# Kernel optimization log

Hardware: AMD Instinct MI355X
Metric: run time of the kernel (lower is better)

The kernel has to match this reference:

```python
import jax, jax.numpy as jnp
import numpy as np

IMAGE_H, IMAGE_W = 256, 704
Z, Y, X = 128, 8, 128
BOUNDS = (-50.0, 50.0, -5.0, 5.0, -50.0, 50.0)
CENTROID = (0.0, 1.0, 0.0)
EPS_MEAN = 1e-6
EPS_DEPTH = 1e-4


def _compose_rt(R, t):
    M = jnp.zeros(R.shape[:-2] + (4, 4), R.dtype)
    M = M.at[..., :3, :3].set(R)
    M = M.at[..., :3, 3].set(t)
    M = M.at[..., 3, 3].set(1.0)
    return M


def _safe_inverse(M):
    R = M[..., :3, :3]
    t = M[..., :3, 3]
    Rt = jnp.swapaxes(R, -1, -2)
    return _compose_rt(Rt, -jnp.einsum('...ij,...j->...i', Rt, t))


def _apply_4x4(M, xyz):
    # M: (...,4,4), xyz: (...,N,3) -> (...,N,3)
    return jnp.einsum('...ij,...nj->...ni', M[..., :3, :3], xyz) + M[..., None, :3, 3]


def _xyz_camA():
    # Mem2Ref of gridcloud3d: x_ref = x_mem*vox + MIN + vox/2 (bounds shifted by centroid)
    xmin = BOUNDS[0] + CENTROID[0]; xmax = BOUNDS[1] + CENTROID[0]
    ymin = BOUNDS[2] + CENTROID[1]; ymax = BOUNDS[3] + CENTROID[1]
    zmin = BOUNDS[4] + CENTROID[2]; zmax = BOUNDS[5] + CENTROID[2]
    vx = (xmax - xmin) / X; vy = (ymax - ymin) / Y; vz = (zmax - zmin) / Z
    zz, yy, xx = jnp.meshgrid(jnp.arange(Z, dtype=jnp.float32),
                              jnp.arange(Y, dtype=jnp.float32),
                              jnp.arange(X, dtype=jnp.float32), indexing='ij')
    x = xx * vx + xmin + vx / 2.0
    y = yy * vy + ymin + vy / 2.0
    z = zz * vz + zmin + vz / 2.0
    return jnp.stack([x, y, z], -1).reshape(Z * Y * X, 3)  # mem order (Z,Y,X)


def _bilinear_sample(img, px, py):
    # img: (C,H,W); px,py: (N,) pixel coords; zeros padding (grid_sample align_corners=False)
    C, H, W = img.shape
    x0 = jnp.floor(px); y0 = jnp.floor(py)
    dx = px - x0; dy = py - y0
    x0i = x0.astype(jnp.int32); y0i = y0.astype(jnp.int32)
    flat = img.reshape(C, H * W)

    def gather(yi, xi, w):
        inb = (xi >= 0) & (xi < W) & (yi >= 0) & (yi < H)
        idx = jnp.clip(yi, 0, H - 1) * W + jnp.clip(xi, 0, W - 1)
        return flat[:, idx] * (w * inb.astype(img.dtype))

    return (gather(y0i, x0i, (1 - dx) * (1 - dy))
            + gather(y0i, x0i + 1, dx * (1 - dy))
            + gather(y0i + 1, x0i, (1 - dx) * dy)
            + gather(y0i + 1, x0i + 1, dx * dy))  # (C,N)


def _forward(cam_feat, camera2ego, cam_intrinsic, conv_w):
    B, S, C, Hf, Wf = cam_feat.shape
    # velo_T_cams = merge_rt(camera2ego R, t); cam0_T_camXs = inv(velo_T_cams[:,0]) @ velo_T_cams
    velo_T_cams = _compose_rt(camera2ego[..., :3, :3], camera2ego[..., :3, 3])
    cam0_T_velo = _safe_inverse(velo_T_cams[:, 0])
    cam0_T_camXs = jnp.einsum('bij,bsjk->bsik', cam0_T_velo, velo_T_cams)
    camXs_T_cam0 = _safe_inverse(cam0_T_camXs)
    # scale_intrinsics with sy = Hf/H*0.284, sx = Wf/W*0.44
    sy = Hf / float(IMAGE_H) * 0.284
    sx = Wf / float(IMAGE_W) * 0.44
    fx = cam_intrinsic[..., 0, 0] * sx
    fy = cam_intrinsic[..., 1, 1] * sy
    cx = cam_intrinsic[..., 0, 2] * sx
    cy = cam_intrinsic[..., 1, 2] * sy
    K = jnp.zeros((B, S, 4, 4), cam_feat.dtype)
    K = K.at[..., 0, 0].set(fx).at[..., 1, 1].set(fy)
    K = K.at[..., 0, 2].set(cx).at[..., 1, 2].set(cy)
    K = K.at[..., 2, 2].set(1.0).at[..., 3, 3].set(1.0)
    pixB_T_cam0 = jnp.einsum('bsij,bsjk->bsik', K, camXs_T_cam0)

    xyz = _xyz_camA()  # (N,3), N = Z*Y*X
    xyz_camB = _apply_4x4(camXs_T_cam0, xyz[None, None])  # (B,S,N,3)
    z_cam = xyz_camB[..., 2]
    xyz_pix = _apply_4x4(pixB_T_cam0, xyz[None, None])
    depth = jnp.maximum(xyz_pix[..., 2], EPS_DEPTH)
    x_pix = xyz_pix[..., 0] / depth
    y_pix = xyz_pix[..., 1] / depth
    valid = ((x_pix > -0.5) & (x_pix < Wf - 0.5)
             & (y_pix > -0.5) & (y_pix < Hf - 0.5)
             & (z_cam > 0.0)).astype(cam_feat.dtype)
    # normalize_grid2d (clamp [-2,2]) then grid_sample align_corners=False unnormalize
    gx = jnp.clip(2.0 * x_pix / (Wf - 1) - 1.0, -2.0, 2.0)
    gy = jnp.clip(2.0 * y_pix / (Hf - 1) - 1.0, -2.0, 2.0)
    px = ((gx + 1.0) * Wf - 1.0) / 2.0
    py = ((gy + 1.0) * Hf - 1.0) / 2.0

    feats = cam_feat.reshape(B * S, C, Hf, Wf)
    vals = jax.vmap(_bilinear_sample)(feats, px.reshape(B * S, -1), py.reshape(B * S, -1))
    vals = vals.reshape(B, S, C, -1) * valid[:, :, None, :]  # (B,S,C,N)
    mask = (jnp.abs(vals) > 0).astype(vals.dtype)
    feat_mem = jnp.sum(vals * mask, axis=1) / (EPS_MEAN + jnp.sum(mask, axis=1))  # (B,C,N)
    feat_mem = feat_mem.reshape(B, C, Z, Y, X)

    # BEV compress: permute(0,1,3,2,4) -> (B, C*Y, Z, X), conv3x3 (no bias), InstanceNorm2d, GELU
    feat_bev = jnp.transpose(feat_mem, (0, 1, 3, 2, 4)).reshape(B, C * Y, Z, X)
    out = jax.lax.conv_general_dilated(feat_bev, conv_w, (1, 1), ((1, 1), (1, 1)),
                                       dimension_numbers=('NCHW', 'OIHW', 'NCHW'))
    mu = jnp.mean(out, axis=(2, 3), keepdims=True)
    var = jnp.var(out, axis=(2, 3), keepdims=True)
    out = (out - mu) / jnp.sqrt(var + 1e-5)
    return jax.nn.gelu(out, approximate=False)


def setup_inputs() -> dict:
    key = jax.random.key(0)
    k1, k2, k3 = jax.random.split(key, 3)
    B, S, C, Hf, Wf = 1, 6, 128, 32, 88
    cam_feat = jax.random.normal(k1, (B, S, C, Hf, Wf), jnp.float32)
    # rigid camera2ego: yaw rotations about the y axis + small translations
    yaws = jnp.arange(S, dtype=jnp.float32) * (2.0 * jnp.pi / S)
    c, s = jnp.cos(yaws), jnp.sin(yaws)
    zr, on = jnp.zeros_like(c), jnp.ones_like(c)
    R = jnp.stack([jnp.stack([c, zr, s], -1),
                   jnp.stack([zr, on, zr], -1),
                   jnp.stack([-s, zr, c], -1)], -2)  # (S,3,3)
    t = jax.random.normal(k2, (S, 3), jnp.float32) * 0.5
    cam2ego = jnp.zeros((B, S, 4, 4), jnp.float32)
    cam2ego = cam2ego.at[0, :, :3, :3].set(R).at[0, :, :3, 3].set(t).at[0, :, 3, 3].set(1.0)
    K = jnp.zeros((B, S, 4, 4), jnp.float32)
    K = K.at[..., 0, 0].set(600.0).at[..., 1, 1].set(600.0)
    K = K.at[..., 0, 2].set(352.0).at[..., 1, 2].set(128.0)
    K = K.at[..., 2, 2].set(1.0).at[..., 3, 3].set(1.0)
    conv_w = jax.random.normal(k3, (128, 128 * Y, 3, 3), jnp.float32) / np.sqrt(128 * Y * 9.0).astype(np.float32)
    return {"cam_feat": cam_feat, "camera2ego": cam2ego, "cam_intrinsic": K, "conv_w": conv_w}


def reference(cam_feat, camera2ego, cam_intrinsic, conv_w):
    return _forward(cam_feat, camera2ego, cam_intrinsic, conv_w)
```

## Files before the change

### kernel.cpp

```cpp
#include <hip/hip_runtime.h>
#include <hip/hip_bf16.h>
#include <math.h>

#define HF 32
#define WF 88
#define NCAM 6
#define CC 128
#define ZD 128
#define YD 8
#define XD 128

using f32x4  = __attribute__((ext_vector_type(4))) float;
using bf16x8 = __attribute__((ext_vector_type(8))) short;
using h2     = __attribute__((ext_vector_type(2))) _Float16;

#if defined(__has_builtin)
#if __has_builtin(__builtin_amdgcn_fdot2)
#define HAVE_FDOT2 1
#endif
#endif
__device__ __forceinline__ float fdot2f(h2 a, h2 b, float c) {
#ifdef HAVE_FDOT2
  return __builtin_amdgcn_fdot2(a, b, c, false);
#else
  return c + (float)a[0] * (float)b[0] + (float)a[1] * (float)b[1];
#endif
}

#define OFF_P    0ull
#define OFF_W    512ull
#define OFF_CAMT (OFF_W + 2359296ull)
#define OFF_F    (OFF_CAMT + 8650752ull)
#define OFF_CONV (OFF_F + 34611200ull)

__global__ __launch_bounds__(256) void k_pre(const float* __restrict__ feat,
                                             const float* __restrict__ conv_w,
                                             const float* __restrict__ cam2ego,
                                             const float* __restrict__ intr,
                                             unsigned* __restrict__ camT2,
                                             __hip_bfloat16* __restrict__ wp,
                                             float* __restrict__ P) {
  __shared__ float tile[128 * 89];
  const int b = blockIdx.x;
  const int t = threadIdx.x;
  if (b < 192) {
    const int s = b >> 5;
    const int hrow = b & 31;
    for (int idx = t; idx < 128 * 88; idx += 256) {
      const int c = idx / 88;
      const int w = idx - c * 88;
      tile[c * 89 + w] = feat[((size_t)(s * CC + c) * HF + hrow) * WF + w];
    }
    __syncthreads();
    unsigned* dst = camT2 + (size_t)(s * 32 + hrow) * 87 * 128;
    for (int idx = t; idx < 87 * 128; idx += 256) {
      const int px = idx >> 7;
      const int c = idx & 127;
      union { _Float16 h[2]; unsigned u; } pr;
      pr.h[0] = (_Float16)tile[c * 89 + px];
      pr.h[1] = (_Float16)tile[c * 89 + px + 1];
      dst[px * 128 + c] = pr.u;
    }
  } else if (b < 704) {
    const int tt = (b - 192) * 256 + t;
    float v[9];
    #pragma unroll
    for (int d = 0; d < 9; d++) v[d] = conv_w[(size_t)tt * 9 + d];
    #pragma unroll
    for (int d = 0; d < 9; d++) wp[(size_t)d * 131072 + tt] = __float2bfloat16(v[d]);
  } else {
    const int s = t;
    if (s >= NCAM) return;
    const float* M0 = cam2ego;
    const float* Ms = cam2ego + s * 16;
    float Rb[9], tb[3];
    for (int i = 0; i < 3; i++)
      for (int j = 0; j < 3; j++) {
        float v = 0.f;
        for (int k = 0; k < 3; k++) v += Ms[k * 4 + i] * M0[k * 4 + j];
        Rb[i * 3 + j] = v;
      }
    for (int i = 0; i < 3; i++) {
      float v = 0.f;
      for (int k = 0; k < 3; k++) v += Ms[k * 4 + i] * (M0[k * 4 + 3] - Ms[k * 4 + 3]);
      tb[i] = v;
    }
    const float* Ks = intr + s * 16;
    const float sx = (float)WF / 704.0f * 0.44f;
    const float sy = (float)HF / 256.0f * 0.284f;
    const float fx = Ks[0] * sx, fy = Ks[5] * sy;
    const float cx = Ks[2] * sx, cy = Ks[6] * sy;
    float* p = P + s * 12;
    for (int j = 0; j < 3; j++) p[j]     = fx * Rb[j]     + cx * Rb[6 + j];
    p[3]  = fx * tb[0] + cx * tb[2];
    for (int j = 0; j < 3; j++) p[4 + j] = fy * Rb[3 + j] + cy * Rb[6 + j];
    p[7]  = fy * tb[1] + cy * tb[2];
    for (int j = 0; j < 3; j++) p[8 + j] = Rb[6 + j];
    p[11] = tb[2];
  }
}

__global__ __launch_bounds__(256) void k2_sample(const unsigned* __restrict__ camT2,
                                                 const float* __restrict__ P,
                                                 __hip_bfloat16* __restrict__ F) {
  const int wv = threadIdx.x >> 6;
  const int l  = threadIdx.x & 63;
  const int cell = blockIdx.x * 4 + wv;
  const int bz = cell / 130;
  const int bx = cell - bz * 130;
  const int zi = bz - 1, xi = bx - 1;
  __hip_bfloat16* Fb = F + (size_t)cell * 1024;

  if (zi < 0 || zi >= ZD || xi < 0 || xi >= XD) {
    const uint4 z4 = {0u, 0u, 0u, 0u};
    *reinterpret_cast<uint4*>(Fb + (2 * l) * 8)     = z4;
    *reinterpret_cast<uint4*>(Fb + (2 * l + 1) * 8) = z4;
    return;
  }

  int offA = 0, offB = 0;
  unsigned pwA = 0, pwB = 0;
  bool vflag = false;
  if (l < 48) {
    const int y = l / 6, s = l - y * 6;
    const float* pp = P + s * 12;
    const float vx = 100.0f / 128.0f;
    const float xw = xi * vx - 50.0f + vx * 0.5f;
    const float zw = zi * vx - 50.0f + vx * 0.5f;
    const float yw = y * 1.25f - 4.0f + 0.625f;
    const float zc = pp[8] * xw + pp[9] * yw + pp[10] * zw + pp[11];
    const float xp = pp[0] * xw + pp[1] * yw + pp[2] * zw + pp[3];
    const float yp = pp[4] * xw + pp[5] * yw + pp[6] * zw + pp[7];
    const float dep = fmaxf(zc, 1e-4f);
    const float pxf = xp / dep, pyf = yp / dep;
    const bool valid = (pxf > -0.5f && pxf < (float)WF - 0.5f &&
                        pyf > -0.5f && pyf < (float)HF - 0.5f && zc > 0.0f);
    const float px = pxf * ((float)WF / (float)(WF - 1)) - 0.5f;
    const float py = pyf * ((float)HF / (float)(HF - 1)) - 0.5f;
    const float fx0 = floorf(px), fy0 = floorf(py);
    const float ddx = px - fx0, ddy = py - fy0;
    const int x0i = (int)fx0, y0i = (int)fy0;
    const float vf = valid ? 1.0f : 0.0f;
    const float wxl = (1.0f - ddx) * vf, wxr = ddx * vf;
    int pxi; float sl, sr;
    if (x0i >= 0 && x0i <= 86)      { pxi = x0i; sl = wxl; sr = wxr; }
    else if (x0i == -1)             { pxi = 0;   sl = wxr; sr = 0.f; }
    else if (x0i == 87)             { pxi = 86;  sl = 0.f; sr = wxl; }
    else                            { pxi = 0;   sl = 0.f; sr = 0.f; }
    const float fA = ((unsigned)y0i < (unsigned)HF) ? (1.0f - ddy) : 0.0f;
    const float fB = ((unsigned)(y0i + 1) < (unsigned)HF) ? ddy : 0.0f;
    const int rowA = min(max(y0i, 0), HF - 1);
    const int rowB = min(max(y0i + 1, 0), HF - 1);
    offA = ((s * HF + rowA) * 87 + pxi) * 128;
    offB = ((s * HF + rowB) * 87 + pxi) * 128;
    union { _Float16 h[2]; unsigned u; } wa, wb;
    wa.h[0] = (_Float16)(sl * fA); wa.h[1] = (_Float16)(sr * fA);
    wb.h[0] = (_Float16)(sl * fB); wb.h[1] = (_Float16)(sr * fB);
    pwA = wa.u; pwB = wb.u;
    vflag = ((sl + sr) * (fA + fB)) > 0.0f;
  }
  const unsigned long long m = __ballot(vflag);

  float accA[8], accB[8];
  #pragma unroll
  for (int y = 0; y < 8; y++) { accA[y] = 0.f; accB[y] = 0.f; }

  #pragma unroll
  for (int y = 0; y < 8; y++) {
    unsigned ms = (unsigned)((m >> (6 * y)) & 63ull);
    const int c = __popc(ms);
    while (ms) {
      const int s = __builtin_ctz(ms);
      ms &= ms - 1;
      const int src = y * 6 + s;
      const int oA = __shfl(offA, src);
      const int oB = __shfl(offB, src);
      const unsigned uwA = (unsigned)__shfl((int)pwA, src);
      const unsigned uwB = (unsigned)__shfl((int)pwB, src);
      const uint2 av = *reinterpret_cast<const uint2*>(camT2 + oA + 2 * l);
      const uint2 bv = *reinterpret_cast<const uint2*>(camT2 + oB + 2 * l);
      const h2 wa = __builtin_bit_cast(h2, uwA);
      const h2 wb = __builtin_bit_cast(h2, uwB);
      accA[y] = fdot2f(__builtin_bit_cast(h2, av.x), wa, accA[y]);
      accB[y] = fdot2f(__builtin_bit_cast(h2, av.y), wa, accB[y]);
      accA[y] = fdot2f(__builtin_bit_cast(h2, bv.x), wb, accA[y]);
      accB[y] = fdot2f(__builtin_bit_cast(h2, bv.y), wb, accB[y]);
    }
    const float inv = 1.0f / (1e-6f + (float)c);
    accA[y] *= inv;
    accB[y] *= inv;
  }

  union { __hip_bfloat16 h[8]; uint4 u; } pA, pB;
  #pragma unroll
  for (int y = 0; y < 8; y++) {
    pA.h[y] = __float2bfloat16(accA[y]);
    pB.h[y] = __float2bfloat16(accB[y]);
  }
  *reinterpret_cast<uint4*>(Fb + (2 * l) * 8)     = pA.u;
  *reinterpret_cast<uint4*>(Fb + (2 * l + 1) * 8) = pB.u;
}

__device__ __forceinline__ void load_lds16(const void* g, void* l) {
  __builtin_amdgcn_global_load_lds(
      (const __attribute__((address_space(1))) unsigned int*)g,
      (__attribute__((address_space(3))) unsigned int*)l, 16, 0, 0);
}

#define K3_NT 72

__global__ __launch_bounds__(512) void k3_gemm(const __hip_bfloat16* __restrict__ F,
                                               const __hip_bfloat16* __restrict__ Wp,
                                               float* __restrict__ out0,
                                               float* __restrict__ out1) {
  const int orig = (blockIdx.x & 7) * 32 + (blockIdx.x >> 3);
  const int z = orig & 127;
  const int h = orig >> 7;
  const int ciH = h << 9;
  const int tid = threadIdx.x;
  const int w = tid >> 6;
  const int l = tid & 63;
  const int kk = w >> 2;
  const int wq = w & 3;
  const int wm = wq >> 1;
  const int wn = wq & 1;
  __shared__ __hip_bfloat16 lds[4][16384];

  f32x4 acc[4][4];
  #pragma unroll
  for (int m = 0; m < 4; m++)
    #pragma unroll
    for (int n = 0; n < 4; n++)
      acc[m][n] = (f32x4){0.f, 0.f, 0.f, 0.f};

  auto stage_A = [&](int kt) {
    const int buf = kt & 3;
    const int d = kt >> 3;
    const int dz = d / 3, dx = d - dz * 3;
    const int ci0 = ciH + ((kt & 7) << 6);
    const int zbase = (z + dz) * 130 + dx;
    #pragma unroll
    for (int i = 0; i < 2; i++) {
      const int n = w * 128 + i * 64 + l;
      const int row = n >> 3;
      const int q = (n & 7) ^ (row & 7);
      const __hip_bfloat16* src = F + ((size_t)(zbase + row) << 10) + ci0 + (q << 3);
      load_lds16(src, &lds[buf][(w * 128 + i * 64) * 8]);
    }
  };
  auto stage_B = [&](int kt) {
    const int buf = kt & 3;
    const int d = kt >> 3;
    const int ci0 = ciH + ((kt & 7) << 6);
    #pragma unroll
    for (int i = 0; i < 2; i++) {
      const int n = w * 128 + i * 64 + l;
      const int co = n >> 3;
      const int q = (n & 7) ^ (co & 7);
      const __hip_bfloat16* src = Wp + ((size_t)d << 17) + ((size_t)co << 10) + ci0 + (q << 3);
      load_lds16(src, &lds[buf][8192 + (w * 128 + i * 64) * 8]);
    }
  };

  const int r16 = l & 15;
  const int hi = l >> 4;
  const int cslot = kk * 4 + hi;

  auto step = [&](int t, bool doStage, int wcode) {
    const int buf = t & 3;
    bf16x8 a[4], b[4];
    #pragma unroll
    for (int m = 0; m < 4; m++) {
      const int r = wm * 64 + m * 16 + r16;
      const int slot = cslot ^ (r & 7);
      a[m] = *reinterpret_cast<const bf16x8*>(&lds[buf][r * 64 + slot * 8]);
    }
    #pragma unroll
    for (int n = 0; n < 2; n++) {
      const int co = wn * 64 + n * 16 + r16;
      const int slot = cslot ^ (co & 7);
      b[n] = *reinterpret_cast<const bf16x8*>(&lds[buf][8192 + co * 64 + slot * 8]);
    }
    if (doStage) stage_A(t + 3);
    __builtin_amdgcn_s_barrier();
    __builtin_amdgcn_s_setprio(1);
    #pragma unroll
    for (int m = 0; m < 4; m++) {
      acc[m][0] = __builtin_amdgcn_mfma_f32_16x16x32_bf16(a[m], b[0], acc[m][0], 0, 0, 0);
      acc[m][1] = __builtin_amdgcn_mfma_f32_16x16x32_bf16(a[m], b[1], acc[m][1], 0, 0, 0);
    }
    __builtin_amdgcn_s_setprio(0);
    __builtin_amdgcn_s_barrier();
    #pragma unroll
    for (int n = 2; n < 4; n++) {
      const int co = wn * 64 + n * 16 + r16;
      const int slot = cslot ^ (co & 7);
      b[n] = *reinterpret_cast<const bf16x8*>(&lds[buf][8192 + co * 64 + slot * 8]);
    }
    if (doStage) stage_B(t + 3);
    __builtin_amdgcn_s_barrier();
    __builtin_amdgcn_s_setprio(1);
    #pragma unroll
    for (int m = 0; m < 4; m++) {
      acc[m][2] = __builtin_amdgcn_mfma_f32_16x16x32_bf16(a[m], b[2], acc[m][2], 0, 0, 0);
      acc[m][3] = __builtin_amdgcn_mfma_f32_16x16x32_bf16(a[m], b[3], acc[m][3], 0, 0, 0);
    }
    __builtin_amdgcn_s_setprio(0);
    if (wcode == 8)      asm volatile("s_waitcnt vmcnt(8)" ::: "memory");
    else if (wcode == 4) asm volatile("s_waitcnt vmcnt(4)" ::: "memory");
    else if (wcode == 0) asm volatile("s_waitcnt vmcnt(0)" ::: "memory");
    __builtin_amdgcn_s_barrier();
  };

  stage_A(0); stage_B(0); stage_A(1); stage_B(1); stage_A(2); stage_B(2);
  asm volatile("s_waitcnt vmcnt(8)" ::: "memory");
  __builtin_amdgcn_s_barrier();

  for (int t = 0; t < K3_NT - 3; ++t) step(t, true, 8);
  step(K3_NT - 3, false, 4);
  step(K3_NT - 2, false, 0);
  step(K3_NT - 1, false, -1);

  float* red = reinterpret_cast<float*>(&lds[0][0]);
  if (kk == 1) {
    float* dst = red + wq * 4096;
    #pragma unroll
    for (int m = 0; m < 4; m++)
      #pragma unroll
      for (int n = 0; n < 4; n++)
        *reinterpret_cast<f32x4*>(&dst[(m * 4 + n) * 256 + l * 4]) = acc[m][n];
  }
  __syncthreads();
  if (kk == 0) {
    const float* srcr = red + wq * 4096;
    float* outP = h ? out1 : out0;
    #pragma unroll
    for (int m = 0; m < 4; m++) {
      const int xr = wm * 64 + m * 16 + hi * 4;
      #pragma unroll
      for (int n = 0; n < 4; n++) {
        f32x4 o = *reinterpret_cast<const f32x4*>(&srcr[(m * 4 + n) * 256 + l * 4]);
        f32x4 r = acc[m][n] + o;
        const int co = wn * 64 + n * 16 + r16;
        *reinterpret_cast<f32x4*>(&outP[((size_t)co << 14) + (z << 7) + xr]) = r;
      }
    }
  }
}

__device__ __forceinline__ float gelu_exact(float x) {
  return 0.5f * x * (1.0f + erff(x * 0.70710678118654752440f));
}

__global__ __launch_bounds__(1024) void k4_ln(const float* __restrict__ c0,
                                              const float* __restrict__ c1,
                                              float* __restrict__ outp) {
  const int co = blockIdx.x;
  const int t = threadIdx.x;
  const float4* p0 = reinterpret_cast<const float4*>(c0 + ((size_t)co << 14));
  const float4* p1 = reinterpret_cast<const float4*>(c1 + ((size_t)co << 14));
  float4 v[4];
  float s = 0.f, s2 = 0.f;
  #pragma unroll
  for (int i = 0; i < 4; i++) {
    float4 a = p0[t + (i << 10)];
    float4 b = p1[t + (i << 10)];
    float4 r;
    r.x = a.x + b.x; r.y = a.y + b.y; r.z = a.z + b.z; r.w = a.w + b.w;
    v[i] = r;
    s  += r.x + r.y + r.z + r.w;
    s2 += r.x * r.x + r.y * r.y + r.z * r.z + r.w * r.w;
  }
  #pragma unroll
  for (int off = 32; off > 0; off >>= 1) {
    s  += __shfl_down(s, off);
    s2 += __shfl_down(s2, off);
  }
  __shared__ float red[32];
  __shared__ float mb[2];
  const int wv = t >> 6, ln = t & 63;
  if (ln == 0) { red[wv] = s; red[wv + 16] = s2; }
  __syncthreads();
  if (t == 0) {
    float S = 0.f, S2 = 0.f;
    #pragma unroll
    for (int i = 0; i < 16; i++) { S += red[i]; S2 += red[i + 16]; }
    float mu = S * (1.0f / 16384.0f);
    float var = S2 * (1.0f / 16384.0f) - mu * mu;
    mb[0] = mu;
    mb[1] = 1.0f / sqrtf(var + 1e-5f);
  }
  __syncthreads();
  const float mu = mb[0], inv = mb[1];
  float4* op = reinterpret_cast<float4*>(outp + ((size_t)co << 14));
  #pragma unroll
  for (int i = 0; i < 4; i++) {
    float4 x = v[i];
    float4 r;
    r.x = gelu_exact((x.x - mu) * inv);
    r.y = gelu_exact((x.y - mu) * inv);
    r.z = gelu_exact((x.z - mu) * inv);
    r.w = gelu_exact((x.w - mu) * inv);
    op[t + (i << 10)] = r;
  }
}

extern "C" void kernel_launch(void* const* d_in, const int* in_sizes, int n_in,
                              void* d_out, int out_size, void* d_ws, size_t ws_size,
                              hipStream_t stream) {
  const float* cam_feat = (const float*)d_in[0];
  const float* cam2ego  = (const float*)d_in[1];
  const float* intr     = (const float*)d_in[2];
  const float* conv_w   = (const float*)d_in[3];
  float* out = (float*)d_out;
  char* ws = (char*)d_ws;

  float*          P     = (float*)(ws + OFF_P);
  __hip_bfloat16* Wp    = (__hip_bfloat16*)(ws + OFF_W);
  unsigned*       camT2 = (unsigned*)(ws + OFF_CAMT);
  __hip_bfloat16* F     = (__hip_bfloat16*)(ws + OFF_F);
  float*          conv0 = (float*)(ws + OFF_CONV);
  float*          conv1 = (float*)(ws + OFF_CAMT);

  hipLaunchKernelGGL(k_pre, dim3(705), dim3(256), 0, stream,
                     cam_feat, conv_w, cam2ego, intr, camT2, Wp, P);
  hipLaunchKernelGGL(k2_sample, dim3(4225), dim3(256), 0, stream, camT2, P, F);
  hipLaunchKernelGGL(k3_gemm, dim3(256), dim3(512), 0, stream, F, Wp, conv0, conv1);
  hipLaunchKernelGGL(k4_ln, dim3(128), dim3(1024), 0, stream, conv0, conv1, out);
}
```

Baseline: 95.69 us.

## Split sampling cells across two waves and software-pipeline gathers

Each grid cell's eight Y levels are now split between two wavefronts, four levels each, and the grid size is doubled. The per-level gather loop uses readlane instead of shuffles and prefetches the next camera's feature rows before accumulating the current one. The aim is more parallelism and overlap of gather latency with the fdot2 work in the bilinear sampling kernel. In exchange each wave stores narrower 8-byte chunks instead of 16-byte ones, and the per-cell projection work is repeated across the two waves.

```diff
diff --git a/kernel.cpp b/kernel.cpp
--- a/kernel.cpp
+++ b/kernel.cpp
@@ -105,24 +105,26 @@
                                                  __hip_bfloat16* __restrict__ F) {
   const int wv = threadIdx.x >> 6;
   const int l  = threadIdx.x & 63;
-  const int cell = blockIdx.x * 4 + wv;
+  const int cell = blockIdx.x * 2 + (wv >> 1);
+  const int yh = wv & 1;
   const int bz = cell / 130;
   const int bx = cell - bz * 130;
   const int zi = bz - 1, xi = bx - 1;
   __hip_bfloat16* Fb = F + (size_t)cell * 1024;
 
   if (zi < 0 || zi >= ZD || xi < 0 || xi >= XD) {
-    const uint4 z4 = {0u, 0u, 0u, 0u};
-    *reinterpret_cast<uint4*>(Fb + (2 * l) * 8)     = z4;
-    *reinterpret_cast<uint4*>(Fb + (2 * l + 1) * 8) = z4;
+    const ushort4 z4 = {0, 0, 0, 0};
+    *reinterpret_cast<ushort4*>(Fb + (2 * l) * 8 + yh * 4)     = z4;
+    *reinterpret_cast<ushort4*>(Fb + (2 * l + 1) * 8 + yh * 4) = z4;
     return;
   }
 
   int offA = 0, offB = 0;
-  unsigned pwA = 0, pwB = 0;
+  int pwA = 0, pwB = 0;
   bool vflag = false;
-  if (l < 48) {
-    const int y = l / 6, s = l - y * 6;
+  if (l < 24) {
+    const int yi = l / 6, s = l - yi * 6;
+    const int y = yh * 4 + yi;
     const float* pp = P + s * 12;
     const float vx = 100.0f / 128.0f;
     const float xw = xi * vx - 50.0f + vx * 0.5f;
@@ -153,7 +155,7 @@
     const int rowB = min(max(y0i + 1, 0), HF - 1);
     offA = ((s * HF + rowA) * 87 + pxi) * 128;
     offB = ((s * HF + rowB) * 87 + pxi) * 128;
-    union { _Float16 h[2]; unsigned u; } wa, wb;
+    union { _Float16 h[2]; int u; } wa, wb;
     wa.h[0] = (_Float16)(sl * fA); wa.h[1] = (_Float16)(sr * fA);
     wb.h[0] = (_Float16)(sl * fB); wb.h[1] = (_Float16)(sr * fB);
     pwA = wa.u; pwB = wb.u;
@@ -161,44 +163,58 @@
   }
   const unsigned long long m = __ballot(vflag);
 
-  float accA[8], accB[8];
-  #pragma unroll
-  for (int y = 0; y < 8; y++) { accA[y] = 0.f; accB[y] = 0.f; }
-
-  #pragma unroll
-  for (int y = 0; y < 8; y++) {
-    unsigned ms = (unsigned)((m >> (6 * y)) & 63ull);
-    const int c = __popc(ms);
-    while (ms) {
-      const int s = __builtin_ctz(ms);
-      ms &= ms - 1;
-      const int src = y * 6 + s;
-      const int oA = __shfl(offA, src);
-      const int oB = __shfl(offB, src);
-      const unsigned uwA = (unsigned)__shfl((int)pwA, src);
-      const unsigned uwB = (unsigned)__shfl((int)pwB, src);
-      const uint2 av = *reinterpret_cast<const uint2*>(camT2 + oA + 2 * l);
-      const uint2 bv = *reinterpret_cast<const uint2*>(camT2 + oB + 2 * l);
+  float accA[4], accB[4];
+  #pragma unroll
+  for (int yi = 0; yi < 4; yi++) {
+    unsigned ms = (unsigned)((m >> (6 * yi)) & 63ull);
+    const float cntf = (float)__popc(ms);
+    float a0 = 0.f, a1 = 0.f;
+    if (ms) {
+      int s = __builtin_ctz(ms); ms &= ms - 1;
+      int src = yi * 6 + s;
+      int oA = __builtin_amdgcn_readlane(offA, src);
+      int oB = __builtin_amdgcn_readlane(offB, src);
+      int uwA = __builtin_amdgcn_readlane(pwA, src);
+      int uwB = __builtin_amdgcn_readlane(pwB, src);
+      uint2 av = *reinterpret_cast<const uint2*>(camT2 + oA + 2 * l);
+      uint2 bv = *reinterpret_cast<const uint2*>(camT2 + oB + 2 * l);
+      while (ms) {
+        int sn = __builtin_ctz(ms); ms &= ms - 1;
+        int srcn = yi * 6 + sn;
+        int oAn = __builtin_amdgcn_readlane(offA, srcn);
+        int oBn = __builtin_amdgcn_readlane(offB, srcn);
+        int uwAn = __builtin_amdgcn_readlane(pwA, srcn);
+        int uwBn = __builtin_amdgcn_readlane(pwB, srcn);
+        uint2 avn = *reinterpret_cast<const uint2*>(camT2 + oAn + 2 * l);
+        uint2 bvn = *reinterpret_cast<const uint2*>(camT2 + oBn + 2 * l);
+        const h2 wa = __builtin_bit_cast(h2, uwA);
+        const h2 wb = __builtin_bit_cast(h2, uwB);
+        a0 = fdot2f(__builtin_bit_cast(h2, av.x), wa, a0);
+        a1 = fdot2f(__builtin_bit_cast(h2, av.y), wa, a1);
+        a0 = fdot2f(__builtin_bit_cast(h2, bv.x), wb, a0);
+        a1 = fdot2f(__builtin_bit_cast(h2, bv.y), wb, a1);
+        av = avn; bv = bvn; uwA = uwAn; uwB = uwBn;
+      }
       const h2 wa = __builtin_bit_cast(h2, uwA);
       const h2 wb = __builtin_bit_cast(h2, uwB);
-      accA[y] = fdot2f(__builtin_bit_cast(h2, av.x), wa, accA[y]);
-      accB[y] = fdot2f(__builtin_bit_cast(h2, av.y), wa, accB[y]);
-      accA[y] = fdot2f(__builtin_bit_cast(h2, bv.x), wb, accA[y]);
-      accB[y] = fdot2f(__builtin_bit_cast(h2, bv.y), wb, accB[y]);
-    }
-    const float inv = 1.0f / (1e-6f + (float)c);
-    accA[y] *= inv;
-    accB[y] *= inv;
-  }
-
-  union { __hip_bfloat16 h[8]; uint4 u; } pA, pB;
-  #pragma unroll
-  for (int y = 0; y < 8; y++) {
-    pA.h[y] = __float2bfloat16(accA[y]);
-    pB.h[y] = __float2bfloat16(accB[y]);
-  }
-  *reinterpret_cast<uint4*>(Fb + (2 * l) * 8)     = pA.u;
-  *reinterpret_cast<uint4*>(Fb + (2 * l + 1) * 8) = pB.u;
+      a0 = fdot2f(__builtin_bit_cast(h2, av.x), wa, a0);
+      a1 = fdot2f(__builtin_bit_cast(h2, av.y), wa, a1);
+      a0 = fdot2f(__builtin_bit_cast(h2, bv.x), wb, a0);
+      a1 = fdot2f(__builtin_bit_cast(h2, bv.y), wb, a1);
+    }
+    const float inv = 1.0f / (1e-6f + cntf);
+    accA[yi] = a0 * inv;
+    accB[yi] = a1 * inv;
+  }
+
+  union { __hip_bfloat16 h[4]; ushort4 u; } pA, pB;
+  #pragma unroll
+  for (int yi = 0; yi < 4; yi++) {
+    pA.h[yi] = __float2bfloat16(accA[yi]);
+    pB.h[yi] = __float2bfloat16(accB[yi]);
+  }
+  *reinterpret_cast<ushort4*>(Fb + (2 * l) * 8 + yh * 4)     = pA.u;
+  *reinterpret_cast<ushort4*>(Fb + (2 * l + 1) * 8 + yh * 4) = pB.u;
 }
 
 __device__ __forceinline__ void load_lds16(const void* g, void* l) {
@@ -424,7 +440,7 @@
 
   hipLaunchKernelGGL(k_pre, dim3(705), dim3(256), 0, stream,
                      cam_feat, conv_w, cam2ego, intr, camT2, Wp, P);
-  hipLaunchKernelGGL(k2_sample, dim3(4225), dim3(256), 0, stream, camT2, P, F);
+  hipLaunchKernelGGL(k2_sample, dim3(8450), dim3(256), 0, stream, camT2, P, F);
   hipLaunchKernelGGL(k3_gemm, dim3(256), dim3(512), 0, stream, F, Wp, conv0, conv1);
   hipLaunchKernelGGL(k4_ln, dim3(128), dim3(1024), 0, stream, conv0, conv1, out);
 }
```

After: 97.24 us. About the same (+1.6%).
